# Kernel optimization log

Hardware: AMD Instinct MI355X
Metric: run time of the kernel (lower is better)

## Reference

```python
import jax, jax.numpy as jnp
import numpy as np

B, T, D = 4, 2048, 1024
H = 16
DH = D // H
BASE = 10000.0


def _rope_tables(seq_len, dim):
    inv_freq = 1.0 / (BASE ** (np.arange(0, dim, 2, dtype=np.float32) / dim))
    pos = np.arange(seq_len, dtype=np.float32)
    freqs = np.outer(pos, inv_freq)            # (T, dim/2)
    emb = np.concatenate([freqs, freqs], -1)   # (T, dim)
    return jnp.asarray(np.cos(emb)), jnp.asarray(np.sin(emb))


def setup_inputs() -> dict:
    key = jax.random.key(0)
    ks = jax.random.split(key, 5)
    s = 1.0 / np.sqrt(D)
    x = jax.random.normal(ks[0], (B, T, D), jnp.float32)
    Wqkv = jax.random.normal(ks[1], (D, 3 * D), jnp.float32) * s
    bqkv = jnp.zeros((3 * D,), jnp.float32)
    Wproj = jax.random.normal(ks[2], (D, D), jnp.float32) * s
    bproj = jnp.zeros((D,), jnp.float32)
    cos, sin = _rope_tables(T, DH)
    return {"x": x, "Wqkv": Wqkv, "bqkv": bqkv, "Wproj": Wproj,
            "bproj": bproj, "cos": cos, "sin": sin}


def _rotate_half(u):
    u1, u2 = jnp.split(u, 2, axis=-1)
    return jnp.concatenate([-u2, u1], axis=-1)


def reference(x, Wqkv, bqkv, Wproj, bproj, cos, sin):
    b, t, d = x.shape
    qkv = x @ Wqkv + bqkv                       # (B, T, 3D)
    qkv = qkv.reshape(b, t, 3, H, DH)           # matches '(three h d)' order
    q, k, v = qkv[:, :, 0], qkv[:, :, 1], qkv[:, :, 2]  # (B, T, H, DH)
    c = cos[None, :, None, :]                   # (1, T, 1, DH)
    s = sin[None, :, None, :]
    q = q * c + _rotate_half(q) * s
    k = k * c + _rotate_half(k) * s
    scale = DH ** -0.5
    attn = jnp.einsum('bthd,bshd->bhts', q, k) * scale   # (B, H, T, T)
    attn = jax.nn.softmax(attn, axis=-1)
    out = jnp.einsum('bhts,bshd->bthd', attn, v)          # (B, T, H, DH)
    out = out.reshape(b, t, d)
    return out @ Wproj + bproj
```

## Files before the change

### kernel.cpp

```cpp
#include <hip/hip_runtime.h>


typedef _Float16 half_t;
typedef _Float16 half8 __attribute__((ext_vector_type(8)));
typedef _Float16 half4v __attribute__((ext_vector_type(4)));
typedef __fp16 fp16x2 __attribute__((ext_vector_type(2)));
typedef float floatx4 __attribute__((ext_vector_type(4)));

#define MFMA_F16 __builtin_amdgcn_mfma_f32_16x16x32_f16

constexpr int Bdim = 4, T = 2048, D = 1024, H = 16, DH = 64;
constexpr int Mrows = Bdim * T;
constexpr int N1 = 3 * D;
constexpr int KD = D;
constexpr int NT2 = KD / 64;

constexpr float QSCALE = 0.125f * 1.4426950408889634f;
constexpr float CSHIFT = 4.0f * 1.4426950408889634f;

__device__ __forceinline__ void gl_lds16(const half_t* g, half_t* l) {
  __builtin_amdgcn_global_load_lds(
      (const __attribute__((address_space(1))) void*)g,
      (__attribute__((address_space(3))) void*)l, 16, 0, 0);
}

__global__ __launch_bounds__(256) void cvt_kernel(const float* __restrict__ s,
                                                  half_t* __restrict__ d, int n4) {
  int i = blockIdx.x * 256 + threadIdx.x;
  if (i < n4) {
    float4 v = ((const float4*)s)[i];
    half4v h;
    h[0] = (half_t)v.x; h[1] = (half_t)v.y; h[2] = (half_t)v.z; h[3] = (half_t)v.w;
    ((half4v*)d)[i] = h;
  }
}

__global__ __launch_bounds__(64) void cvt_transpose(const float* __restrict__ W,
                                                    half_t* __restrict__ Wt,
                                                    int Kr, int Nc) {
  __shared__ half_t Th[32][36];
  const int l = threadIdx.x;
  const int n0 = blockIdx.x * 32, k0 = blockIdx.y * 32;
#pragma unroll
  for (int i = 0; i < 4; ++i) {
    int kk = (l >> 3) + i * 8;
    int nn4 = (l & 7) * 4;
    float4 v = *(const float4*)(W + (size_t)(k0 + kk) * Nc + n0 + nn4);
    half4v h;
    h[0] = (half_t)v.x; h[1] = (half_t)v.y; h[2] = (half_t)v.z; h[3] = (half_t)v.w;
    *(half4v*)&Th[kk][nn4] = h;
  }
  __syncthreads();
#pragma unroll
  for (int i = 0; i < 4; ++i) {
    int nn = (l >> 3) + i * 8;
    int kk4 = (l & 7) * 4;
    half4v h;
#pragma unroll
    for (int j = 0; j < 4; ++j) h[j] = Th[kk4 + j][nn];
    *(half4v*)(Wt + (size_t)(n0 + nn) * Kr + k0 + kk4) = h;
  }
}

struct GemmFrags {
  half8 af[4][2], bf[4][2];
};

#define GEMM8_BODY(X_, Wt_, BNBLK)                                              \
  __shared__ half_t As[2][256 * 64];                                            \
  __shared__ half_t Bs[2][128 * 64];                                            \
  const int tid = threadIdx.x;                                                  \
  const int lane = tid & 63, wv = tid >> 6;                                     \
  const int wm = wv >> 1, wn = wv & 1;                                          \
  const int qd = lane >> 4, ln = lane & 15;                                     \
  const half_t* Asrc[4]; const half_t* Bsrc[2];                                 \
  int destA[4], destB[2];                                                       \
  _Pragma("unroll")                                                             \
  for (int p = 0; p < 4; ++p) {                                                 \
    int c = tid + p * 512, r = c >> 3, s = c & 7, g = s ^ (r & 7);              \
    Asrc[p] = X_ + (size_t)(bm * 256 + r) * KD + g * 8;                         \
    destA[p] = c * 8;                                                           \
  }                                                                             \
  _Pragma("unroll")                                                             \
  for (int p = 0; p < 2; ++p) {                                                 \
    int c = tid + p * 512, r = c >> 3, s = c & 7, g = s ^ (r & 7);              \
    Bsrc[p] = Wt_ + (size_t)(bn * 128 + r) * KD + g * 8;                        \
    destB[p] = c * 8;                                                           \
  }                                                                             \
  int offA[4][2], offB[4][2];                                                   \
  _Pragma("unroll")                                                             \
  for (int mi = 0; mi < 4; ++mi) {                                              \
    int r = wm * 64 + mi * 16 + ln;                                             \
    _Pragma("unroll")                                                           \
    for (int ks = 0; ks < 2; ++ks)                                              \
      offA[mi][ks] = r * 64 + (((ks * 4 + qd) ^ (r & 7)) << 3);                 \
  }                                                                             \
  _Pragma("unroll")                                                             \
  for (int ni = 0; ni < 4; ++ni) {                                              \
    int r = wn * 64 + ni * 16 + ln;                                             \
    _Pragma("unroll")                                                           \
    for (int ks = 0; ks < 2; ++ks)                                              \
      offB[ni][ks] = r * 64 + (((ks * 4 + qd) ^ (r & 7)) << 3);                 \
  }                                                                             \
  floatx4 acc[4][4] = {};                                                       \
  _Pragma("unroll")                                                             \
  for (int t0 = 0; t0 < 2; ++t0) {                                              \
    _Pragma("unroll")                                                           \
    for (int p = 0; p < 4; ++p) gl_lds16(Asrc[p] + t0 * 64, &As[t0][0] + destA[p]); \
    _Pragma("unroll")                                                           \
    for (int p = 0; p < 2; ++p) gl_lds16(Bsrc[p] + t0 * 64, &Bs[t0][0] + destB[p]); \
  }                                                                             \
  asm volatile("s_waitcnt vmcnt(6)" ::: "memory");                              \
  __builtin_amdgcn_s_barrier();                                                 \
  for (int t = 0; t < NT2; ++t) {                                               \
    const int bsel = t & 1;                                                     \
    const half_t* Ab = &As[bsel][0];                                            \
    const half_t* Bb = &Bs[bsel][0];                                            \
    half_t* An = &As[bsel][0];                                                  \
    half_t* Bn = &Bs[bsel][0];                                                  \
    const bool st = (t + 2 < NT2);                                              \
    GemmFrags f;                                                                \
    _Pragma("unroll")                                                           \
    for (int mi = 0; mi < 4; ++mi)                                              \
      _Pragma("unroll")                                                         \
      for (int ks = 0; ks < 2; ++ks) f.af[mi][ks] = *(const half8*)&Ab[offA[mi][ks]]; \
    _Pragma("unroll")                                                           \
    for (int ni = 0; ni < 4; ++ni)                                              \
      _Pragma("unroll")                                                         \
      for (int ks = 0; ks < 2; ++ks) f.bf[ni][ks] = *(const half8*)&Bb[offB[ni][ks]]; \
    asm volatile("s_waitcnt lgkmcnt(0)" ::: "memory");                          \
    __builtin_amdgcn_sched_barrier(0);                                          \
    __builtin_amdgcn_s_barrier();                                               \
    __builtin_amdgcn_s_setprio(1);                                              \
    _Pragma("unroll")                                                           \
    for (int mi = 0; mi < 2; ++mi)                                              \
      _Pragma("unroll")                                                         \
      for (int ni = 0; ni < 4; ++ni)                                            \
        acc[mi][ni] = MFMA_F16(f.af[mi][0], f.bf[ni][0], acc[mi][ni], 0, 0, 0); \
    __builtin_amdgcn_s_setprio(0);                                              \
    __builtin_amdgcn_s_barrier();                                               \
    if (st) { gl_lds16(Asrc[0] + (t + 2) * 64, An + destA[0]);                  \
              gl_lds16(Asrc[1] + (t + 2) * 64, An + destA[1]); }                \
    __builtin_amdgcn_s_barrier();                                               \
    __builtin_amdgcn_s_setprio(1);                                              \
    _Pragma("unroll")                                                           \
    for (int mi = 2; mi < 4; ++mi)                                              \
      _Pragma("unroll")                                                         \
      for (int ni = 0; ni < 4; ++ni)                                            \
        acc[mi][ni] = MFMA_F16(f.af[mi][0], f.bf[ni][0], acc[mi][ni], 0, 0, 0); \
    __builtin_amdgcn_s_setprio(0);                                              \
    __builtin_amdgcn_s_barrier();                                               \
    if (st) { gl_lds16(Asrc[2] + (t + 2) * 64, An + destA[2]);                  \
              gl_lds16(Asrc[3] + (t + 2) * 64, An + destA[3]); }                \
    __builtin_amdgcn_s_barrier();                                               \
    __builtin_amdgcn_s_setprio(1);                                              \
    _Pragma("unroll")                                                           \
    for (int mi = 0; mi < 2; ++mi)                                              \
      _Pragma("unroll")                                                         \
      for (int ni = 0; ni < 4; ++ni)                                            \
        acc[mi][ni] = MFMA_F16(f.af[mi][1], f.bf[ni][1], acc[mi][ni], 0, 0, 0); \
    __builtin_amdgcn_s_setprio(0);                                              \
    __builtin_amdgcn_s_barrier();                                               \
    if (st) { gl_lds16(Bsrc[0] + (t + 2) * 64, Bn + destB[0]);                  \
              gl_lds16(Bsrc[1] + (t + 2) * 64, Bn + destB[1]); }                \
    __builtin_amdgcn_s_barrier();                                               \
    __builtin_amdgcn_s_setprio(1);                                              \
    _Pragma("unroll")                                                           \
    for (int mi = 2; mi < 4; ++mi)                                              \
      _Pragma("unroll")                                                         \
      for (int ni = 0; ni < 4; ++ni)                                            \
        acc[mi][ni] = MFMA_F16(f.af[mi][1], f.bf[ni][1], acc[mi][ni], 0, 0, 0); \
    __builtin_amdgcn_s_setprio(0);                                              \
    if (st) asm volatile("s_waitcnt vmcnt(6)" ::: "memory");                    \
    else    asm volatile("s_waitcnt vmcnt(0)" ::: "memory");                    \
    __builtin_amdgcn_s_barrier();                                               \
  }

__global__ __launch_bounds__(512, 1) void gemm_qkv_rope(
    const half_t* __restrict__ X, const half_t* __restrict__ Wt,
    const float* __restrict__ bias, const float* __restrict__ cosT,
    const float* __restrict__ sinT,
    half_t* __restrict__ Q, half_t* __restrict__ K, half_t* __restrict__ V) {
  const int flat = blockIdx.y * 24 + blockIdx.x;
  const int swzb = (flat & 7) * 96 + (flat >> 3);
  const int bn = swzb % 24, bm = swzb / 24;

  GEMM8_BODY(X, Wt, 24)

  const int n0 = bn * 128 + wn * 64;
  const int sreg = n0 >> 10;
  const int h = (n0 & 1023) >> 6;
  float bv[4];
#pragma unroll
  for (int ni = 0; ni < 4; ++ni) bv[ni] = bias[n0 + ni * 16 + ln];

  if (sreg == 2) {
#pragma unroll
    for (int mi = 0; mi < 4; ++mi) {
      int m0 = bm * 256 + wm * 64 + mi * 16 + qd * 4;
      int b = m0 >> 11, t0 = m0 & (T - 1);
#pragma unroll
      for (int ni = 0; ni < 4; ++ni) {
        int dh = ni * 16 + ln;
        half4v hv;
#pragma unroll
        for (int r = 0; r < 4; ++r) hv[r] = (half_t)(acc[mi][ni][r] + bv[ni]);
        *(half4v*)(V + ((size_t)(b * H + h) * DH + dh) * T + t0) = hv;
      }
    }
  } else {
    const float qscale = (sreg == 0) ? QSCALE : 1.0f;
    half_t* OUT = (sreg == 0) ? Q : K;
#pragma unroll
    for (int mi = 0; mi < 4; ++mi) {
#pragma unroll
      for (int r = 0; r < 4; ++r) {
        int m = bm * 256 + wm * 64 + mi * 16 + qd * 4 + r;
        int b = m >> 11, t = m & (T - 1);
        float v0 = acc[mi][0][r] + bv[0];
        float v1 = acc[mi][1][r] + bv[1];
        float v2 = acc[mi][2][r] + bv[2];
        float v3 = acc[mi][3][r] + bv[3];
        float c0 = cosT[t * 64 + ln],      s0 = sinT[t * 64 + ln];
        float c1 = cosT[t * 64 + 16 + ln], s1 = sinT[t * 64 + 16 + ln];
        float c2 = cosT[t * 64 + 32 + ln], s2 = sinT[t * 64 + 32 + ln];
        float c3 = cosT[t * 64 + 48 + ln], s3 = sinT[t * 64 + 48 + ln];
        float o0 = v0 * c0 - v2 * s0;
        float o1 = v1 * c1 - v3 * s1;
        float o2 = v2 * c2 + v0 * s2;
        float o3 = v3 * c3 + v1 * s3;
        size_t base = ((size_t)(b * H + h) * T + t) * DH;
        OUT[base + 0 * 16 + ln] = (half_t)(o0 * qscale);
        OUT[base + 1 * 16 + ln] = (half_t)(o1 * qscale);
        OUT[base + 2 * 16 + ln] = (half_t)(o2 * qscale);
        OUT[base + 3 * 16 + ln] = (half_t)(o3 * qscale);
      }
    }
  }
}

__global__ __launch_bounds__(512, 1) void gemm_proj(
    const half_t* __restrict__ X, const half_t* __restrict__ Wt,
    const float* __restrict__ bias, float* __restrict__ OUTF) {
  const int flat = blockIdx.y * 8 + blockIdx.x;
  const int swzb = (flat & 7) * 32 + (flat >> 3);
  const int bn = swzb % 8, bm = swzb / 8;

  GEMM8_BODY(X, Wt, 8)

  const int n0 = bn * 128 + wn * 64;
  float bv[4];
#pragma unroll
  for (int ni = 0; ni < 4; ++ni) bv[ni] = bias[n0 + ni * 16 + ln];
#pragma unroll
  for (int mi = 0; mi < 4; ++mi) {
#pragma unroll
    for (int r = 0; r < 4; ++r) {
      int m = bm * 256 + wm * 64 + mi * 16 + qd * 4 + r;
#pragma unroll
      for (int ni = 0; ni < 4; ++ni)
        OUTF[(size_t)m * D + n0 + ni * 16 + ln] = acc[mi][ni][r] + bv[ni];
    }
  }
}

__global__ __launch_bounds__(512, 4) void flash_attn(
    const half_t* __restrict__ Q, const half_t* __restrict__ K,
    const half_t* __restrict__ Vt, half_t* __restrict__ AO) {
  __shared__ __align__(16) half_t Klds[2][64 * 64];
  __shared__ __align__(16) half_t Vlds[2][64 * 64];
  __shared__ __align__(16) half_t Pw[8][32 * 64];
  const int tid = threadIdx.x;
  const int lane = tid & 63, wv = tid >> 6;
  const int qd = lane >> 4, ln = lane & 15;
  const int flat = blockIdx.y * 8 + blockIdx.x;
  const int swzb = (flat & 7) * 64 + (flat >> 3);
  const int bh = swzb >> 3;
  const int q0 = (swzb & 7) * 256 + wv * 32;
  const half_t* Qb = Q + (size_t)bh * T * DH;
  const half_t* Kb = K + (size_t)bh * T * DH;
  const half_t* Vb = Vt + (size_t)bh * DH * T;
  half_t* Pq = Pw[wv];
  const int swz = (ln & 7) << 3;
  const fp16x2 one2 = {(__fp16)1.0f, (__fp16)1.0f};

  const int sr = tid >> 3, sc8 = (tid & 7) << 3;
  const int stoff = sr * 64 + (sc8 ^ ((sr & 7) << 3));
  const half_t* Kg = Kb + (size_t)sr * DH + sc8;
  const half_t* Vg = Vb + (size_t)sr * T + sc8;

  half8 qf[2][2];
#pragma unroll
  for (int mi = 0; mi < 2; ++mi)
#pragma unroll
    for (int ks = 0; ks < 2; ++ks)
      qf[mi][ks] = *(const half8*)(Qb + (size_t)(q0 + mi * 16 + ln) * DH + ks * 32 + qd * 8);

  floatx4 Oacc[2][4] = {};
  float La[2] = {0.f, 0.f};
  float Lb2[2] = {0.f, 0.f};

  half8 kreg = *(const half8*)Kg;
  half8 vreg = *(const half8*)Vg;
  *(half8*)&Klds[0][stoff] = kreg;
  *(half8*)&Vlds[0][stoff] = vreg;
  kreg = *(const half8*)(Kg + (size_t)64 * DH);
  vreg = *(const half8*)(Vg + 64);

  for (int t = 0; t < T / 64; ++t) {
    __syncthreads();
    if (t + 1 < T / 64) {
      *(half8*)&Klds[(t + 1) & 1][stoff] = kreg;
      *(half8*)&Vlds[(t + 1) & 1][stoff] = vreg;
      if (t + 2 < T / 64) {
        kreg = *(const half8*)(Kg + (size_t)(t + 2) * 64 * DH);
        vreg = *(const half8*)(Vg + (t + 2) * 64);
      }
    }
    const half_t* Kc = Klds[t & 1];
    const half_t* Vc = Vlds[t & 1];

#pragma unroll
    for (int ni = 0; ni < 4; ++ni) {
      floatx4 s4[2] = {floatx4{-CSHIFT, -CSHIFT, -CSHIFT, -CSHIFT},
                       floatx4{-CSHIFT, -CSHIFT, -CSHIFT, -CSHIFT}};
#pragma unroll
      for (int ks = 0; ks < 2; ++ks) {
        int krow = ni * 16 + ln;
        half8 kf = *(const half8*)&Kc[krow * 64 + (((ks * 32) | (qd * 8)) ^ swz)];
        __builtin_amdgcn_s_setprio(1);
#pragma unroll
        for (int mi = 0; mi < 2; ++mi)
          s4[mi] = MFMA_F16(kf, qf[mi][ks], s4[mi], 0, 0, 0);
        __builtin_amdgcn_s_setprio(0);
      }
#pragma unroll
      for (int mi = 0; mi < 2; ++mi) {
        float p0 = __builtin_amdgcn_exp2f(s4[mi][0]);
        float p1 = __builtin_amdgcn_exp2f(s4[mi][1]);
        float p2 = __builtin_amdgcn_exp2f(s4[mi][2]);
        float p3 = __builtin_amdgcn_exp2f(s4[mi][3]);
        fp16x2 h01 = __builtin_amdgcn_cvt_pkrtz(p0, p1);
        fp16x2 h23 = __builtin_amdgcn_cvt_pkrtz(p2, p3);
        La[mi]  = __builtin_amdgcn_fdot2(h01, one2, La[mi], false);
        Lb2[mi] = __builtin_amdgcn_fdot2(h23, one2, Lb2[mi], false);
        union { half4v h4; fp16x2 h2[2]; } pu;
        pu.h2[0] = h01; pu.h2[1] = h23;
        int row = mi * 16 + ln;
        int chunk = ni * 16 + ((qd >> 1) << 3);
        int low = (qd & 1) << 2;
        *(half4v*)&Pq[row * 64 + (chunk ^ swz) + low] = pu.h4;
      }
    }

#pragma unroll
    for (int ks = 0; ks < 2; ++ks) {
      half8 pf[2];
#pragma unroll
      for (int mi = 0; mi < 2; ++mi)
        pf[mi] = *(const half8*)&Pq[(mi * 16 + ln) * 64 + (((ks * 32) | (qd * 8)) ^ swz)];
#pragma unroll
      for (int di = 0; di < 4; ++di) {
        half8 vf = *(const half8*)&Vc[(di * 16 + ln) * 64 + (((ks * 32) | (qd * 8)) ^ swz)];
        __builtin_amdgcn_s_setprio(1);
#pragma unroll
        for (int mi = 0; mi < 2; ++mi)
          Oacc[mi][di] = MFMA_F16(pf[mi], vf, Oacc[mi][di], 0, 0, 0);
        __builtin_amdgcn_s_setprio(0);
      }
    }
  }

  float Ls[2];
#pragma unroll
  for (int mi = 0; mi < 2; ++mi) {
    Ls[mi] = La[mi] + Lb2[mi];
    Ls[mi] += __shfl_xor(Ls[mi], 16);
    Ls[mi] += __shfl_xor(Ls[mi], 32);
  }

  const int b = bh >> 4, h = bh & 15;
#pragma unroll
  for (int mi = 0; mi < 2; ++mi) {
#pragma unroll
    for (int r = 0; r < 4; ++r) {
      float invL = 1.f / __shfl(Ls[mi], qd * 4 + r);
      int t = q0 + mi * 16 + qd * 4 + r;
      size_t base = ((size_t)b * T + t) * D + h * DH;
#pragma unroll
      for (int di = 0; di < 4; ++di)
        AO[base + di * 16 + ln] = (half_t)(Oacc[mi][di][r] * invL);
    }
  }
}

extern "C" void kernel_launch(void* const* d_in, const int* in_sizes, int n_in,
                              void* d_out, int out_size, void* d_ws, size_t ws_size,
                              hipStream_t stream) {
  const float* x     = (const float*)d_in[0];
  const float* Wqkv  = (const float*)d_in[1];
  const float* bqkv  = (const float*)d_in[2];
  const float* Wproj = (const float*)d_in[3];
  const float* bproj = (const float*)d_in[4];
  const float* cosT  = (const float*)d_in[5];
  const float* sinT  = (const float*)d_in[6];
  float* out = (float*)d_out;

  half_t* xh      = (half_t*)d_ws;
  half_t* Wqkvt   = xh + (size_t)Mrows * KD;
  half_t* Wprojt  = Wqkvt + (size_t)KD * N1;
  half_t* Qb      = Wprojt + (size_t)D * D;
  half_t* Kb      = Qb + (size_t)Bdim * H * T * DH;
  half_t* Vb      = Kb + (size_t)Bdim * H * T * DH;
  half_t* AO      = xh;

  cvt_kernel<<<(Mrows * KD / 4 + 255) / 256, 256, 0, stream>>>(x, xh, Mrows * KD / 4);
  cvt_transpose<<<dim3(N1 / 32, KD / 32), 64, 0, stream>>>(Wqkv, Wqkvt, KD, N1);
  cvt_transpose<<<dim3(D / 32, KD / 32), 64, 0, stream>>>(Wproj, Wprojt, KD, D);

  gemm_qkv_rope<<<dim3(N1 / 128, Mrows / 256), 512, 0, stream>>>(
      xh, Wqkvt, bqkv, cosT, sinT, Qb, Kb, Vb);
  flash_attn<<<dim3(T / 256, Bdim * H), 512, 0, stream>>>(Qb, Kb, Vb, AO);
  gemm_proj<<<dim3(D / 128, Mrows / 256), 512, 0, stream>>>(AO, Wprojt, bproj, out);
}
```

Measured before the change: 287.0 us.

## Replace GEMM mainloop with 3-stage BK=32 pipeline using 256-thread blocks

Rewrites the shared GEMM body used by the QKV+RoPE and projection kernels. The 512-thread, double-buffered BK=64 loop with swizzled LDS and interleaved loads is replaced by a 256-thread, triple-buffered BK=32 loop. Each wave now computes a 128x64 tile with 8x4 accumulators, and 2 blocks per CU are allowed. The aim is simpler prefetch and higher occupancy, but the unswizzled LDS layout risks bank conflicts and each wave needs more registers.

Measured after the change: 317.8 us. +10.7%, slower.

```diff
diff --git a/kernel.cpp b/kernel.cpp
--- a/kernel.cpp
+++ b/kernel.cpp
@@ -13,7 +13,7 @@
 constexpr int Mrows = Bdim * T;
 constexpr int N1 = 3 * D;
 constexpr int KD = D;
-constexpr int NT2 = KD / 64;
+constexpr int NT = KD / 32;
 
 constexpr float QSCALE = 0.125f * 1.4426950408889634f;
 constexpr float CSHIFT = 4.0f * 1.4426950408889634f;
@@ -62,121 +62,74 @@
   }
 }
 
-struct GemmFrags {
-  half8 af[4][2], bf[4][2];
-};
-
-#define GEMM8_BODY(X_, Wt_, BNBLK)                                              \
-  __shared__ half_t As[2][256 * 64];                                            \
-  __shared__ half_t Bs[2][128 * 64];                                            \
+#define GEMM_BIG_BODY(X_, Wt_)                                                  \
+  __shared__ half_t As[3 * 256 * 32];                                           \
+  __shared__ half_t Bs[3 * 128 * 32];                                           \
   const int tid = threadIdx.x;                                                  \
   const int lane = tid & 63, wv = tid >> 6;                                     \
   const int wm = wv >> 1, wn = wv & 1;                                          \
   const int qd = lane >> 4, ln = lane & 15;                                     \
-  const half_t* Asrc[4]; const half_t* Bsrc[2];                                 \
-  int destA[4], destB[2];                                                       \
+  floatx4 acc[8][4] = {};                                                       \
   _Pragma("unroll")                                                             \
-  for (int p = 0; p < 4; ++p) {                                                 \
-    int c = tid + p * 512, r = c >> 3, s = c & 7, g = s ^ (r & 7);              \
-    Asrc[p] = X_ + (size_t)(bm * 256 + r) * KD + g * 8;                         \
-    destA[p] = c * 8;                                                           \
-  }                                                                             \
-  _Pragma("unroll")                                                             \
-  for (int p = 0; p < 2; ++p) {                                                 \
-    int c = tid + p * 512, r = c >> 3, s = c & 7, g = s ^ (r & 7);              \
-    Bsrc[p] = Wt_ + (size_t)(bn * 128 + r) * KD + g * 8;                        \
-    destB[p] = c * 8;                                                           \
-  }                                                                             \
-  int offA[4][2], offB[4][2];                                                   \
-  _Pragma("unroll")                                                             \
-  for (int mi = 0; mi < 4; ++mi) {                                              \
-    int r = wm * 64 + mi * 16 + ln;                                             \
+  for (int pt = 0; pt < 2; ++pt) {                                              \
     _Pragma("unroll")                                                           \
-    for (int ks = 0; ks < 2; ++ks)                                              \
-      offA[mi][ks] = r * 64 + (((ks * 4 + qd) ^ (r & 7)) << 3);                 \
-  }                                                                             \
-  _Pragma("unroll")                                                             \
-  for (int ni = 0; ni < 4; ++ni) {                                              \
-    int r = wn * 64 + ni * 16 + ln;                                             \
+    for (int p = 0; p < 4; ++p) {                                               \
+      int c = tid + p * 256;                                                    \
+      int row = c >> 2, col = (c & 3) << 3;                                     \
+      gl_lds16(X_ + (size_t)(bm * 256 + row) * KD + pt * 32 + col,              \
+               As + pt * 8192 + c * 8);                                         \
+    }                                                                           \
     _Pragma("unroll")                                                           \
-    for (int ks = 0; ks < 2; ++ks)                                              \
-      offB[ni][ks] = r * 64 + (((ks * 4 + qd) ^ (r & 7)) << 3);                 \
-  }                                                                             \
-  floatx4 acc[4][4] = {};                                                       \
-  _Pragma("unroll")                                                             \
-  for (int t0 = 0; t0 < 2; ++t0) {                                              \
-    _Pragma("unroll")                                                           \
-    for (int p = 0; p < 4; ++p) gl_lds16(Asrc[p] + t0 * 64, &As[t0][0] + destA[p]); \
-    _Pragma("unroll")                                                           \
-    for (int p = 0; p < 2; ++p) gl_lds16(Bsrc[p] + t0 * 64, &Bs[t0][0] + destB[p]); \
+    for (int p = 0; p < 2; ++p) {                                               \
+      int c = tid + p * 256;                                                    \
+      int row = c >> 2, col = (c & 3) << 3;                                     \
+      gl_lds16(Wt_ + (size_t)(bn * 128 + row) * KD + pt * 32 + col,             \
+               Bs + pt * 4096 + c * 8);                                         \
+    }                                                                           \
   }                                                                             \
   asm volatile("s_waitcnt vmcnt(6)" ::: "memory");                              \
   __builtin_amdgcn_s_barrier();                                                 \
-  for (int t = 0; t < NT2; ++t) {                                               \
-    const int bsel = t & 1;                                                     \
-    const half_t* Ab = &As[bsel][0];                                            \
-    const half_t* Bb = &Bs[bsel][0];                                            \
-    half_t* An = &As[bsel][0];                                                  \
-    half_t* Bn = &Bs[bsel][0];                                                  \
-    const bool st = (t + 2 < NT2);                                              \
-    GemmFrags f;                                                                \
-    _Pragma("unroll")                                                           \
-    for (int mi = 0; mi < 4; ++mi)                                              \
+  int rd = 0, st = 2;                                                           \
+  for (int t = 0; t < NT; ++t) {                                                \
+    if (t + 2 < NT) {                                                           \
       _Pragma("unroll")                                                         \
-      for (int ks = 0; ks < 2; ++ks) f.af[mi][ks] = *(const half8*)&Ab[offA[mi][ks]]; \
+      for (int p = 0; p < 4; ++p) {                                             \
+        int c = tid + p * 256;                                                  \
+        int row = c >> 2, col = (c & 3) << 3;                                   \
+        gl_lds16(X_ + (size_t)(bm * 256 + row) * KD + (t + 2) * 32 + col,       \
+                 As + st * 8192 + c * 8);                                       \
+      }                                                                         \
+      _Pragma("unroll")                                                         \
+      for (int p = 0; p < 2; ++p) {                                             \
+        int c = tid + p * 256;                                                  \
+        int row = c >> 2, col = (c & 3) << 3;                                   \
+        gl_lds16(Wt_ + (size_t)(bn * 128 + row) * KD + (t + 2) * 32 + col,      \
+                 Bs + st * 4096 + c * 8);                                       \
+      }                                                                         \
+    }                                                                           \
+    const half_t* Ab = As + rd * 8192;                                          \
+    const half_t* Bb = Bs + rd * 4096;                                          \
+    half8 bf[4];                                                                \
     _Pragma("unroll")                                                           \
     for (int ni = 0; ni < 4; ++ni)                                              \
-      _Pragma("unroll")                                                         \
-      for (int ks = 0; ks < 2; ++ks) f.bf[ni][ks] = *(const half8*)&Bb[offB[ni][ks]]; \
-    asm volatile("s_waitcnt lgkmcnt(0)" ::: "memory");                          \
-    __builtin_amdgcn_sched_barrier(0);                                          \
-    __builtin_amdgcn_s_barrier();                                               \
-    __builtin_amdgcn_s_setprio(1);                                              \
+      bf[ni] = *(const half8*)&Bb[(wn * 64 + ni * 16 + ln) * 32 + qd * 8];      \
     _Pragma("unroll")                                                           \
-    for (int mi = 0; mi < 2; ++mi)                                              \
+    for (int mi = 0; mi < 8; ++mi) {                                            \
+      half8 af = *(const half8*)&Ab[(wm * 128 + mi * 16 + ln) * 32 + qd * 8];   \
+      __builtin_amdgcn_s_setprio(1);                                            \
       _Pragma("unroll")                                                         \
       for (int ni = 0; ni < 4; ++ni)                                            \
-        acc[mi][ni] = MFMA_F16(f.af[mi][0], f.bf[ni][0], acc[mi][ni], 0, 0, 0); \
-    __builtin_amdgcn_s_setprio(0);                                              \
+        acc[mi][ni] = MFMA_F16(af, bf[ni], acc[mi][ni], 0, 0, 0);               \
+      __builtin_amdgcn_s_setprio(0);                                            \
+    }                                                                           \
+    if (t + 2 < NT) asm volatile("s_waitcnt vmcnt(6)" ::: "memory");            \
+    else            asm volatile("s_waitcnt vmcnt(0)" ::: "memory");            \
     __builtin_amdgcn_s_barrier();                                               \
-    if (st) { gl_lds16(Asrc[0] + (t + 2) * 64, An + destA[0]);                  \
-              gl_lds16(Asrc[1] + (t + 2) * 64, An + destA[1]); }                \
-    __builtin_amdgcn_s_barrier();                                               \
-    __builtin_amdgcn_s_setprio(1);                                              \
-    _Pragma("unroll")                                                           \
-    for (int mi = 2; mi < 4; ++mi)                                              \
-      _Pragma("unroll")                                                         \
-      for (int ni = 0; ni < 4; ++ni)                                            \
-        acc[mi][ni] = MFMA_F16(f.af[mi][0], f.bf[ni][0], acc[mi][ni], 0, 0, 0); \
-    __builtin_amdgcn_s_setprio(0);                                              \
-    __builtin_amdgcn_s_barrier();                                               \
-    if (st) { gl_lds16(Asrc[2] + (t + 2) * 64, An + destA[2]);                  \
-              gl_lds16(Asrc[3] + (t + 2) * 64, An + destA[3]); }                \
-    __builtin_amdgcn_s_barrier();                                               \
-    __builtin_amdgcn_s_setprio(1);                                              \
-    _Pragma("unroll")                                                           \
-    for (int mi = 0; mi < 2; ++mi)                                              \
-      _Pragma("unroll")                                                         \
-      for (int ni = 0; ni < 4; ++ni)                                            \
-        acc[mi][ni] = MFMA_F16(f.af[mi][1], f.bf[ni][1], acc[mi][ni], 0, 0, 0); \
-    __builtin_amdgcn_s_setprio(0);                                              \
-    __builtin_amdgcn_s_barrier();                                               \
-    if (st) { gl_lds16(Bsrc[0] + (t + 2) * 64, Bn + destB[0]);                  \
-              gl_lds16(Bsrc[1] + (t + 2) * 64, Bn + destB[1]); }                \
-    __builtin_amdgcn_s_barrier();                                               \
-    __builtin_amdgcn_s_setprio(1);                                              \
-    _Pragma("unroll")                                                           \
-    for (int mi = 2; mi < 4; ++mi)                                              \
-      _Pragma("unroll")                                                         \
-      for (int ni = 0; ni < 4; ++ni)                                            \
-        acc[mi][ni] = MFMA_F16(f.af[mi][1], f.bf[ni][1], acc[mi][ni], 0, 0, 0); \
-    __builtin_amdgcn_s_setprio(0);                                              \
-    if (st) asm volatile("s_waitcnt vmcnt(6)" ::: "memory");                    \
-    else    asm volatile("s_waitcnt vmcnt(0)" ::: "memory");                    \
-    __builtin_amdgcn_s_barrier();                                               \
-  }
-
-__global__ __launch_bounds__(512, 1) void gemm_qkv_rope(
+    rd = (rd == 2) ? 0 : rd + 1;                                                \
+    st = (st == 2) ? 0 : st + 1;                                                \
+  }
+
+__global__ __launch_bounds__(256, 2) void gemm_qkv_rope(
     const half_t* __restrict__ X, const half_t* __restrict__ Wt,
     const float* __restrict__ bias, const float* __restrict__ cosT,
     const float* __restrict__ sinT,
@@ -185,7 +138,7 @@
   const int swzb = (flat & 7) * 96 + (flat >> 3);
   const int bn = swzb % 24, bm = swzb / 24;
 
-  GEMM8_BODY(X, Wt, 24)
+  GEMM_BIG_BODY(X, Wt)
 
   const int n0 = bn * 128 + wn * 64;
   const int sreg = n0 >> 10;
@@ -196,8 +149,8 @@
 
   if (sreg == 2) {
 #pragma unroll
-    for (int mi = 0; mi < 4; ++mi) {
-      int m0 = bm * 256 + wm * 64 + mi * 16 + qd * 4;
+    for (int mi = 0; mi < 8; ++mi) {
+      int m0 = bm * 256 + wm * 128 + mi * 16 + qd * 4;
       int b = m0 >> 11, t0 = m0 & (T - 1);
 #pragma unroll
       for (int ni = 0; ni < 4; ++ni) {
@@ -212,10 +165,10 @@
     const float qscale = (sreg == 0) ? QSCALE : 1.0f;
     half_t* OUT = (sreg == 0) ? Q : K;
 #pragma unroll
-    for (int mi = 0; mi < 4; ++mi) {
+    for (int mi = 0; mi < 8; ++mi) {
 #pragma unroll
       for (int r = 0; r < 4; ++r) {
-        int m = bm * 256 + wm * 64 + mi * 16 + qd * 4 + r;
+        int m = bm * 256 + wm * 128 + mi * 16 + qd * 4 + r;
         int b = m >> 11, t = m & (T - 1);
         float v0 = acc[mi][0][r] + bv[0];
         float v1 = acc[mi][1][r] + bv[1];
@@ -239,24 +192,24 @@
   }
 }
 
-__global__ __launch_bounds__(512, 1) void gemm_proj(
+__global__ __launch_bounds__(256, 2) void gemm_proj(
     const half_t* __restrict__ X, const half_t* __restrict__ Wt,
     const float* __restrict__ bias, float* __restrict__ OUTF) {
   const int flat = blockIdx.y * 8 + blockIdx.x;
   const int swzb = (flat & 7) * 32 + (flat >> 3);
   const int bn = swzb % 8, bm = swzb / 8;
 
-  GEMM8_BODY(X, Wt, 8)
+  GEMM_BIG_BODY(X, Wt)
 
   const int n0 = bn * 128 + wn * 64;
   float bv[4];
 #pragma unroll
   for (int ni = 0; ni < 4; ++ni) bv[ni] = bias[n0 + ni * 16 + ln];
 #pragma unroll
-  for (int mi = 0; mi < 4; ++mi) {
+  for (int mi = 0; mi < 8; ++mi) {
 #pragma unroll
     for (int r = 0; r < 4; ++r) {
-      int m = bm * 256 + wm * 64 + mi * 16 + qd * 4 + r;
+      int m = bm * 256 + wm * 128 + mi * 16 + qd * 4 + r;
 #pragma unroll
       for (int ni = 0; ni < 4; ++ni)
         OUTF[(size_t)m * D + n0 + ni * 16 + ln] = acc[mi][ni][r] + bv[ni];
@@ -418,8 +371,8 @@
   cvt_transpose<<<dim3(N1 / 32, KD / 32), 64, 0, stream>>>(Wqkv, Wqkvt, KD, N1);
   cvt_transpose<<<dim3(D / 32, KD / 32), 64, 0, stream>>>(Wproj, Wprojt, KD, D);
 
-  gemm_qkv_rope<<<dim3(N1 / 128, Mrows / 256), 512, 0, stream>>>(
+  gemm_qkv_rope<<<dim3(N1 / 128, Mrows / 256), 256, 0, stream>>>(
       xh, Wqkvt, bqkv, cosT, sinT, Qb, Kb, Vb);
   flash_attn<<<dim3(T / 256, Bdim * H), 512, 0, stream>>>(Qb, Kb, Vb, AO);
-  gemm_proj<<<dim3(D / 128, Mrows / 256), 512, 0, stream>>>(AO, Wprojt, bproj, out);
-}
+  gemm_proj<<<dim3(D / 128, Mrows / 256), 256, 0, stream>>>(AO, Wprojt, bproj, out);
+}
```
